# Performance work log

Measured on AMD Instinct MI355X. Metric: run time of the kernel, lower is better.

Reference implementation:

```python
import jax, jax.numpy as jnp
import numpy as np

B, H, S, DK = 2, 16, 2048, 128


def setup_inputs() -> dict:
    key = jax.random.key(0)
    kq, kk, kv = jax.random.split(key, 3)
    return {
        "queries": jax.random.normal(kq, (B, H, S, DK), dtype=jnp.float32),
        "keys": jax.random.normal(kk, (B, H, S, DK), dtype=jnp.float32),
        "values": jax.random.normal(kv, (B, H, S, DK), dtype=jnp.float32),
        "d_k": DK,
    }


def reference(queries, keys, values, d_k):
    # scores: [B, H, Sq, Sk] = Q @ K^T / sqrt(d_k)
    scale = 1.0 / np.sqrt(float(d_k)).astype(np.float32)
    scores = jnp.einsum("bhqd,bhkd->bhqk", queries, keys) * scale
    weights = jax.nn.softmax(scores, axis=-1)
    return jnp.einsum("bhqk,bhkd->bhqd", weights, values)
```

## Files before the change

kernel.cpp:

```cpp
#include <hip/hip_runtime.h>
#include <hip/hip_bf16.h>

#define SREF 2048
#define DHEAD 128
#define KVBLK 64
#define NTHREADS 256
#define NTILES (SREF / KVBLK)
#define PSTR 72
#define QSCALE 0.12751743f
#define THRLOG 8.0f

typedef short bf16x8 __attribute__((ext_vector_type(8)));
typedef float f32x4 __attribute__((ext_vector_type(4)));
typedef float f32x16 __attribute__((ext_vector_type(16)));

typedef const __attribute__((address_space(1))) void* gas_t;
typedef __attribute__((address_space(3))) void* las_t;

__device__ __forceinline__ ushort f2bf(float x) {
    unsigned u = __builtin_bit_cast(unsigned, x);
    u += 0x7fffu + ((u >> 16) & 1u);
    return (ushort)(u >> 16);
}

__device__ __forceinline__ float fexp2(float x) {
#if __has_builtin(__builtin_amdgcn_exp2f)
    return __builtin_amdgcn_exp2f(x);
#else
    return exp2f(x);
#endif
}

__device__ __forceinline__ unsigned cvtpk(float lo, float hi) {
    unsigned r;
    asm("v_cvt_pk_bf16_f32 %0, %1, %2" : "=v"(r) : "v"(lo), "v"(hi));
    return r;
}

__global__ __launch_bounds__(NTHREADS) void preconv_kernel(
    const float* __restrict__ K, const float* __restrict__ V,
    ushort* __restrict__ Kb, ushort* __restrict__ VTb)
{
    __shared__ ushort T[DHEAD * PSTR];
    const int t  = threadIdx.x;
    const int bh = blockIdx.y;
    const int s0 = blockIdx.x * KVBLK;
    const size_t base = (size_t)bh * SREF * DHEAD;

    const float* kb = K + base + (size_t)s0 * DHEAD;
    ushort* kout = Kb + base + (size_t)s0 * DHEAD;
    #pragma unroll
    for (int i = 0; i < 8; ++i) {
        int idx = t + i * NTHREADS;
        float4 f = *(const float4*)(kb + idx * 4);
        ushort4 h; h.x = f2bf(f.x); h.y = f2bf(f.y); h.z = f2bf(f.z); h.w = f2bf(f.w);
        *(ushort4*)(kout + idx * 4) = h;
    }

    const float* vb = V + base + (size_t)s0 * DHEAD;
    #pragma unroll
    for (int i = 0; i < 8; ++i) {
        const int key = (t & 31) + 32 * (i & 1);
        const int d4  = (t >> 5) + 8 * (i >> 1);
        float4 f = *(const float4*)(vb + key * DHEAD + d4 * 4);
        T[(d4 * 4 + 0) * PSTR + key] = f2bf(f.x);
        T[(d4 * 4 + 1) * PSTR + key] = f2bf(f.y);
        T[(d4 * 4 + 2) * PSTR + key] = f2bf(f.z);
        T[(d4 * 4 + 3) * PSTR + key] = f2bf(f.w);
    }
    __syncthreads();

    ushort* vt = VTb + (size_t)bh * DHEAD * SREF + s0;
    #pragma unroll
    for (int i = 0; i < 4; ++i) {
        int idx = t + i * NTHREADS;
        int d = idx >> 3;
        int c = (idx & 7) * 8;
        bf16x8 v = *(const bf16x8*)&T[d * PSTR + c];
        *(bf16x8*)(vt + (size_t)d * SREF + c) = v;
    }
}

__device__ __forceinline__ void softmax_step(
    f32x16& s0, f32x16& s1, float& mrun, float& lsumh,
    f32x16* acc, bf16x8* pa)
{
    float m0[8];
    #pragma unroll
    for (int i = 0; i < 8; ++i)
        m0[i] = fmaxf(fmaxf(s0[i], s0[i + 8]), fmaxf(s1[i], s1[i + 8]));
    float pmax = fmaxf(fmaxf(fmaxf(m0[0], m0[1]), fmaxf(m0[2], m0[3])),
                       fmaxf(fmaxf(m0[4], m0[5]), fmaxf(m0[6], m0[7])));
    pmax = fmaxf(pmax, __shfl_xor(pmax, 32));

    if (!__all(pmax <= mrun + THRLOG)) {
        const float mnew  = fmaxf(mrun, pmax);
        const float alpha = fexp2(mrun - mnew);
        mrun = mnew;
        lsumh *= alpha;
        #pragma unroll
        for (int db = 0; db < 4; ++db)
            #pragma unroll
            for (int i = 0; i < 16; ++i) acc[db][i] *= alpha;
    }

    float r0 = 0.f, r1 = 0.f, r2 = 0.f, r3 = 0.f;
    #pragma unroll
    for (int i = 0; i < 16; i += 4) {
        s0[i]   = fexp2(s0[i]   - mrun); r0 += s0[i];
        s0[i+1] = fexp2(s0[i+1] - mrun); r1 += s0[i+1];
        s0[i+2] = fexp2(s0[i+2] - mrun); r2 += s0[i+2];
        s0[i+3] = fexp2(s0[i+3] - mrun); r3 += s0[i+3];
    }
    #pragma unroll
    for (int i = 0; i < 16; i += 4) {
        s1[i]   = fexp2(s1[i]   - mrun); r0 += s1[i];
        s1[i+1] = fexp2(s1[i+1] - mrun); r1 += s1[i+1];
        s1[i+2] = fexp2(s1[i+2] - mrun); r2 += s1[i+2];
        s1[i+3] = fexp2(s1[i+3] - mrun); r3 += s1[i+3];
    }
    lsumh += (r0 + r1) + (r2 + r3);

    #pragma unroll
    for (int kb = 0; kb < 2; ++kb) {
        #pragma unroll
        for (int c = 0; c < 2; ++c) {
            unsigned x0, x1, y0, y1;
            if (kb == 0) {
                x0 = cvtpk(s0[8*c+0], s0[8*c+1]); x1 = cvtpk(s0[8*c+2], s0[8*c+3]);
                y0 = cvtpk(s0[8*c+4], s0[8*c+5]); y1 = cvtpk(s0[8*c+6], s0[8*c+7]);
            } else {
                x0 = cvtpk(s1[8*c+0], s1[8*c+1]); x1 = cvtpk(s1[8*c+2], s1[8*c+3]);
                y0 = cvtpk(s1[8*c+4], s1[8*c+5]); y1 = cvtpk(s1[8*c+6], s1[8*c+7]);
            }
            asm volatile("v_permlane32_swap_b32 %0, %1" : "+v"(x0), "+v"(y0));
            asm volatile("v_permlane32_swap_b32 %0, %1" : "+v"(x1), "+v"(y1));
            union { unsigned u[4]; bf16x8 v; } U;
            U.u[0] = x0; U.u[1] = x1; U.u[2] = y0; U.u[3] = y1;
            pa[kb * 2 + c] = U.v;
        }
    }
}

__global__ __launch_bounds__(NTHREADS, 2) void attn_fwd_kernel(
    const float* __restrict__ Q, const ushort* __restrict__ Kb,
    const ushort* __restrict__ VTb, float* __restrict__ O)
{
    __shared__ __align__(16) char smem[67584];

    const int t    = threadIdx.x;
    const int lane = t & 63;
    const int wv   = t >> 6;
    const int hi   = lane >> 5;
    const int q5   = lane & 31;
    const int swz  = (lane & 7) << 4;

    const int bh = blockIdx.y;
    const int q0 = blockIdx.x * 128;
    const size_t base = (size_t)bh * SREF * DHEAD;

    bf16x8 qf[8];
    {
        const float* qrow = Q + base + (size_t)(q0 + wv * 32 + q5) * DHEAD;
        #pragma unroll
        for (int dk = 0; dk < 8; ++dk) {
            const int d0 = dk * 16 + hi * 8;
            float4 a = *(const float4*)(qrow + d0);
            float4 b = *(const float4*)(qrow + d0 + 4);
            bf16x8 f;
            f[0] = (short)f2bf(a.x * QSCALE); f[1] = (short)f2bf(a.y * QSCALE);
            f[2] = (short)f2bf(a.z * QSCALE); f[3] = (short)f2bf(a.w * QSCALE);
            f[4] = (short)f2bf(b.x * QSCALE); f[5] = (short)f2bf(b.y * QSCALE);
            f[6] = (short)f2bf(b.z * QSCALE); f[7] = (short)f2bf(b.w * QSCALE);
            qf[dk] = f;
        }
    }

    const char* ksrcb = (const char*)(Kb + base);
    const char* vsrcb = (const char*)(VTb + (size_t)bh * DHEAD * SREF);

    const int kbaseL = q5 * 256 + ((hi * 16) ^ swz);
    const int vbaseL = q5 * 128 + ((hi * 16) ^ swz);

#define KOFF(b) ((b) * 16384)
#define VOFF(b) (32768 + (b) * 16384)

#define STAGE_K(b, kv0) do {                                                    \
    const char* kt_ = ksrcb + (size_t)(kv0) * (DHEAD * 2);                      \
    _Pragma("unroll")                                                           \
    for (int i_ = 0; i_ < 4; ++i_) {                                            \
        int L_ = t * 16 + i_ * 4096;                                            \
        int r_ = L_ >> 8;                                                       \
        __builtin_amdgcn_global_load_lds(                                       \
            (gas_t)(const void*)(kt_ + (L_ ^ ((r_ & 7) << 4))),                 \
            (las_t)(void*)(smem + KOFF(b) + L_), 16, 0, 0);                     \
    }                                                                           \
} while (0)

#define STAGE_V(b, kv0) do {                                                    \
    const char* vt_ = vsrcb + (size_t)(kv0) * 2;                                \
    _Pragma("unroll")                                                           \
    for (int i_ = 0; i_ < 4; ++i_) {                                            \
        int L_ = t * 16 + i_ * 4096;                                            \
        int d_ = L_ >> 7;                                                       \
        int c_ = L_ & 127;                                                      \
        __builtin_amdgcn_global_load_lds(                                       \
            (gas_t)(const void*)(vt_ + (size_t)d_ * (SREF * 2) + (c_ ^ ((d_ & 7) << 4))), \
            (las_t)(void*)(smem + VOFF(b) + L_), 16, 0, 0);                     \
    }                                                                           \
} while (0)

#define QK_REGION(sd0, sd1, kO_) do {                                           \
    _Pragma("unroll")                                                           \
    for (int i_ = 0; i_ < 16; ++i_) { sd0[i_] = 0.f; sd1[i_] = 0.f; }           \
    _Pragma("unroll")                                                           \
    for (int dk_ = 0; dk_ < 8; ++dk_) {                                         \
        bf16x8 kf0 = *(const bf16x8*)(smem + (kO_) + (kbaseL ^ (dk_ << 5)));    \
        sd0 = __builtin_amdgcn_mfma_f32_32x32x16_bf16(kf0, qf[dk_], sd0, 0, 0, 0); \
        bf16x8 kf1 = *(const bf16x8*)(smem + (kO_) + 8192 + (kbaseL ^ (dk_ << 5))); \
        sd1 = __builtin_amdgcn_mfma_f32_32x32x16_bf16(kf1, qf[dk_], sd1, 0, 0, 0); \
    }                                                                           \
} while (0)

#define PV_REGION(pa_, vO_) do {                                                \
    __builtin_amdgcn_s_setprio(1);                                              \
    _Pragma("unroll")                                                           \
    for (int db_ = 0; db_ < 4; ++db_) {                                         \
        _Pragma("unroll")                                                       \
        for (int ks_ = 0; ks_ < 4; ++ks_) {                                     \
            bf16x8 vf = *(const bf16x8*)(smem + (vO_) + db_ * 4096 + (vbaseL ^ (ks_ << 5))); \
            acc[db_] = __builtin_amdgcn_mfma_f32_32x32x16_bf16(vf, pa_[ks_], acc[db_], 0, 0, 0); \
        }                                                                       \
    }                                                                           \
    __builtin_amdgcn_s_setprio(0);                                              \
} while (0)

#define PHASE_SYNC() do {                                                       \
    asm volatile("s_waitcnt vmcnt(0)" ::: "memory");                            \
    __builtin_amdgcn_s_barrier();                                               \
    __builtin_amdgcn_sched_barrier(0);                                          \
} while (0)

    float mrun = -1e30f, lsumh = 0.0f;
    f32x16 acc[4];
    #pragma unroll
    for (int db = 0; db < 4; ++db)
        #pragma unroll
        for (int i = 0; i < 16; ++i) acc[db][i] = 0.0f;

    f32x16 sA0, sA1, sB0, sB1;
    bf16x8 pa[4];

    STAGE_K(0, 0);
    STAGE_K(1, KVBLK);
    STAGE_V(0, 0);
    asm volatile("s_waitcnt vmcnt(16)" ::: "memory");
    __builtin_amdgcn_s_barrier();
    __builtin_amdgcn_sched_barrier(0);
    QK_REGION(sA0, sA1, KOFF(0));

    for (int u = 0; u < 15; ++u) {
        const int t0 = 2 * u;
        PHASE_SYNC();
        STAGE_K(0, (t0 + 2) * KVBLK);
        STAGE_V(1, (t0 + 1) * KVBLK);
        softmax_step(sA0, sA1, mrun, lsumh, acc, pa);
        QK_REGION(sB0, sB1, KOFF(1));
        PV_REGION(pa, VOFF(0));
        PHASE_SYNC();
        STAGE_K(1, (t0 + 3) * KVBLK);
        STAGE_V(0, (t0 + 2) * KVBLK);
        softmax_step(sB0, sB1, mrun, lsumh, acc, pa);
        QK_REGION(sA0, sA1, KOFF(0));
        PV_REGION(pa, VOFF(1));
    }
    PHASE_SYNC();
    STAGE_V(1, 31 * KVBLK);
    softmax_step(sA0, sA1, mrun, lsumh, acc, pa);
    QK_REGION(sB0, sB1, KOFF(1));
    PV_REGION(pa, VOFF(0));
    PHASE_SYNC();
    softmax_step(sB0, sB1, mrun, lsumh, acc, pa);
    PV_REGION(pa, VOFF(1));

    __syncthreads();

    const float lsum = lsumh + __shfl_xor(lsumh, 32);
    const float inv  = 1.0f / lsum;
    const int eb = wv * 16896;
    #pragma unroll
    for (int db = 0; db < 4; ++db) {
        #pragma unroll
        for (int c = 0; c < 4; ++c) {
            f32x4 v;
            v[0] = acc[db][4*c+0] * inv;
            v[1] = acc[db][4*c+1] * inv;
            v[2] = acc[db][4*c+2] * inv;
            v[3] = acc[db][4*c+3] * inv;
            *(f32x4*)(smem + eb + q5 * 528 + db * 128 + c * 32 + hi * 16) = v;
        }
    }
    #pragma unroll
    for (int i = 0; i < 16; ++i) {
        const int flat  = lane + i * 64;
        const int row   = flat >> 5;
        const int chunk = flat & 31;
        f32x4 v = *(const f32x4*)(smem + eb + row * 528 + chunk * 16);
        *(f32x4*)(O + base + (size_t)(q0 + wv * 32 + row) * DHEAD + chunk * 4) = v;
    }
#undef STAGE_K
#undef STAGE_V
#undef QK_REGION
#undef PV_REGION
#undef PHASE_SYNC
#undef KOFF
#undef VOFF
}

__global__ __launch_bounds__(NTHREADS) void attn_fwd_fallback(
    const float* __restrict__ Q, const float* __restrict__ K,
    const float* __restrict__ V, float* __restrict__ O)
{
    __shared__ ushort Ksh[KVBLK * 136];
    __shared__ ushort Vsh[DHEAD * 72];
    __shared__ ushort Psh[4][16 * PSTR];

    const int t    = threadIdx.x;
    const int lane = t & 63;
    const int wv   = t >> 6;
    const int lq   = lane & 15;
    const int kh   = lane >> 4;

    const int bh = blockIdx.y;
    const int q0 = blockIdx.x * 64;
    const size_t base = (size_t)bh * SREF * DHEAD;

    const float scale = 0.08838834764831845f;
    bf16x8 qf[4];
    {
        const float* qrow = Q + base + (size_t)(q0 + wv * 16 + lq) * DHEAD;
        #pragma unroll
        for (int kk = 0; kk < 4; ++kk) {
            const int d0 = kk * 32 + kh * 8;
            float4 a = *(const float4*)(qrow + d0);
            float4 b = *(const float4*)(qrow + d0 + 4);
            bf16x8 f;
            f[0] = (short)f2bf(a.x * scale); f[1] = (short)f2bf(a.y * scale);
            f[2] = (short)f2bf(a.z * scale); f[3] = (short)f2bf(a.w * scale);
            f[4] = (short)f2bf(b.x * scale); f[5] = (short)f2bf(b.y * scale);
            f[6] = (short)f2bf(b.z * scale); f[7] = (short)f2bf(b.w * scale);
            qf[kk] = f;
        }
    }

    float mrun[4], lrun[4];
    f32x4 acc_o[8];
    #pragma unroll
    for (int r = 0; r < 4; ++r) { mrun[r] = -1e30f; lrun[r] = 0.0f; }
    #pragma unroll
    for (int db = 0; db < 8; ++db) acc_o[db] = (f32x4){0.f, 0.f, 0.f, 0.f};

    for (int kv0 = 0; kv0 < SREF; kv0 += KVBLK) {
        __syncthreads();
        const float* kbase = K + base + (size_t)kv0 * DHEAD;
        #pragma unroll
        for (int i = 0; i < 8; ++i) {
            const int idx = t + i * NTHREADS;
            const int row = idx >> 5;
            const int c4  = idx & 31;
            float4 f = *(const float4*)(kbase + row * DHEAD + c4 * 4);
            ushort4 h;
            h.x = f2bf(f.x); h.y = f2bf(f.y); h.z = f2bf(f.z); h.w = f2bf(f.w);
            *(ushort4*)&Ksh[row * 136 + c4 * 4] = h;
        }
        const float* vbase = V + base + (size_t)kv0 * DHEAD;
        #pragma unroll
        for (int i = 0; i < 8; ++i) {
            const int key = (t & 31) + 32 * (i & 1);
            const int d4  = (t >> 5) + 8 * (i >> 1);
            float4 f = *(const float4*)(vbase + key * DHEAD + d4 * 4);
            Vsh[(d4 * 4 + 0) * 72 + key] = f2bf(f.x);
            Vsh[(d4 * 4 + 1) * 72 + key] = f2bf(f.y);
            Vsh[(d4 * 4 + 2) * 72 + key] = f2bf(f.z);
            Vsh[(d4 * 4 + 3) * 72 + key] = f2bf(f.w);
        }
        __syncthreads();

        f32x4 accs[4];
        #pragma unroll
        for (int nb = 0; nb < 4; ++nb) accs[nb] = (f32x4){0.f, 0.f, 0.f, 0.f};
        #pragma unroll
        for (int kk = 0; kk < 4; ++kk) {
            #pragma unroll
            for (int nb = 0; nb < 4; ++nb) {
                bf16x8 kf = *(const bf16x8*)&Ksh[(nb * 16 + lq) * 136 + kk * 32 + kh * 8];
                accs[nb] = __builtin_amdgcn_mfma_f32_16x16x32_bf16(qf[kk], kf, accs[nb], 0, 0, 0);
            }
        }

        float ps[4][4];
        #pragma unroll
        for (int r = 0; r < 4; ++r) {
            float v = fmaxf(fmaxf(accs[0][r], accs[1][r]), fmaxf(accs[2][r], accs[3][r]));
            #pragma unroll
            for (int mk = 1; mk < 16; mk <<= 1) v = fmaxf(v, __shfl_xor(v, mk));
            const float mnew  = fmaxf(mrun[r], v);
            const float alpha = __expf(mrun[r] - mnew);
            mrun[r] = mnew;
            float rs = 0.0f;
            #pragma unroll
            for (int nb = 0; nb < 4; ++nb) {
                const float p = __expf(accs[nb][r] - mnew);
                ps[nb][r] = p;
                rs += p;
            }
            #pragma unroll
            for (int mk = 1; mk < 16; mk <<= 1) rs += __shfl_xor(rs, mk);
            lrun[r] = lrun[r] * alpha + rs;
            #pragma unroll
            for (int db = 0; db < 8; ++db) acc_o[db][r] *= alpha;
        }

        #pragma unroll
        for (int nb = 0; nb < 4; ++nb)
            #pragma unroll
            for (int r = 0; r < 4; ++r)
                Psh[wv][(kh * 4 + r) * PSTR + nb * 16 + lq] = f2bf(ps[nb][r]);

        #pragma unroll
        for (int ks = 0; ks < 2; ++ks) {
            bf16x8 pa = *(const bf16x8*)&Psh[wv][lq * PSTR + ks * 32 + kh * 8];
            #pragma unroll
            for (int db = 0; db < 8; ++db) {
                bf16x8 vf = *(const bf16x8*)&Vsh[(db * 16 + lq) * 72 + ks * 32 + kh * 8];
                acc_o[db] = __builtin_amdgcn_mfma_f32_16x16x32_bf16(pa, vf, acc_o[db], 0, 0, 0);
            }
        }
    }

    #pragma unroll
    for (int r = 0; r < 4; ++r) {
        const float inv = 1.0f / lrun[r];
        float* orow = O + base + (size_t)(q0 + wv * 16 + kh * 4 + r) * DHEAD;
        #pragma unroll
        for (int db = 0; db < 8; ++db)
            orow[db * 16 + lq] = acc_o[db][r] * inv;
    }
}

extern "C" void kernel_launch(void* const* d_in, const int* in_sizes, int n_in,
                              void* d_out, int out_size, void* d_ws, size_t ws_size,
                              hipStream_t stream) {
    const float* Q = (const float*)d_in[0];
    const float* K = (const float*)d_in[1];
    const float* V = (const float*)d_in[2];
    float* O = (float*)d_out;
    const int BH = in_sizes[0] / (SREF * DHEAD);
    const size_t nel = (size_t)BH * SREF * DHEAD;

    if (ws_size >= 2 * nel * sizeof(ushort)) {
        ushort* Kb  = (ushort*)d_ws;
        ushort* VTb = Kb + nel;
        preconv_kernel<<<dim3(SREF / KVBLK, BH), NTHREADS, 0, stream>>>(K, V, Kb, VTb);
        attn_fwd_kernel<<<dim3(SREF / 128, BH), NTHREADS, 0, stream>>>(Q, Kb, VTb, O);
    } else {
        attn_fwd_fallback<<<dim3(SREF / 64, BH), NTHREADS, 0, stream>>>(Q, K, V, O);
    }
}
```

Before: 104.4 us.

## Restructure attention kernel into 8-wave ping-pong with two wave groups

The main attention kernel goes from 4 waves handling 128 queries to 8 waves handling 256 queries, split into two groups of four. While one group runs its QK and PV matrix work, the other runs softmax, and barriers swap the roles. This aims to overlap MFMA work with softmax exponentials and to halve K/V staging traffic per query. The LDS layout changes to a 16-row swizzle with interleaved V, the grid order becomes (BH, seq) for better L2 locality, and the epilogue is serialized into three rounds because LDS is shrunk. In exchange, register pressure at 512 threads is higher and the grid has fewer blocks, which may hurt occupancy.

```diff
diff --git a/kernel.cpp b/kernel.cpp
--- a/kernel.cpp
+++ b/kernel.cpp
@@ -5,7 +5,8 @@
 #define DHEAD 128
 #define KVBLK 64
 #define NTHREADS 256
-#define NTILES (SREF / KVBLK)
+#define ATHREADS 512
+#define NT (SREF / KVBLK)
 #define PSTR 72
 #define QSCALE 0.12751743f
 #define THRLOG 8.0f
@@ -44,7 +45,7 @@
     __shared__ ushort T[DHEAD * PSTR];
     const int t  = threadIdx.x;
     const int bh = blockIdx.y;
-    const int s0 = blockIdx.x * KVBLK;
+    const int s0 = blockIdx.x * 64;
     const size_t base = (size_t)bh * SREF * DHEAD;
 
     const float* kb = K + base + (size_t)s0 * DHEAD;
@@ -142,21 +143,22 @@
     }
 }
 
-__global__ __launch_bounds__(NTHREADS, 2) void attn_fwd_kernel(
+__global__ __launch_bounds__(ATHREADS, 2) void attn_fwd_kernel(
     const float* __restrict__ Q, const ushort* __restrict__ Kb,
     const ushort* __restrict__ VTb, float* __restrict__ O)
 {
-    __shared__ __align__(16) char smem[67584];
+    __shared__ __align__(16) char smem[65536];
 
     const int t    = threadIdx.x;
     const int lane = t & 63;
     const int wv   = t >> 6;
+    const int g    = wv >> 2;
     const int hi   = lane >> 5;
     const int q5   = lane & 31;
-    const int swz  = (lane & 7) << 4;
-
-    const int bh = blockIdx.y;
-    const int q0 = blockIdx.x * 128;
+    const int sw   = (q5 & 15) << 4;
+
+    const int bh = blockIdx.x;
+    const int q0 = blockIdx.y * 256;
     const size_t base = (size_t)bh * SREF * DHEAD;
 
     bf16x8 qf[8];
@@ -179,67 +181,68 @@
     const char* ksrcb = (const char*)(Kb + base);
     const char* vsrcb = (const char*)(VTb + (size_t)bh * DHEAD * SREF);
 
-    const int kbaseL = q5 * 256 + ((hi * 16) ^ swz);
-    const int vbaseL = q5 * 128 + ((hi * 16) ^ swz);
-
-#define KOFF(b) ((b) * 16384)
-#define VOFF(b) (32768 + (b) * 16384)
-
-#define STAGE_K(b, kv0) do {                                                    \
-    const char* kt_ = ksrcb + (size_t)(kv0) * (DHEAD * 2);                      \
+    const int kread = q5 * 256 + ((hi * 16) ^ sw);
+    const int vread = q5 * 256 + ((hi * 16) ^ sw);
+
+#define STAGE_K(tt) do {                                                        \
+    const char* kt_ = ksrcb + (size_t)(tt) * 16384;                             \
     _Pragma("unroll")                                                           \
-    for (int i_ = 0; i_ < 4; ++i_) {                                            \
-        int L_ = t * 16 + i_ * 4096;                                            \
+    for (int i_ = 0; i_ < 2; ++i_) {                                            \
+        int L_ = t * 16 + i_ * 8192;                                            \
         int r_ = L_ >> 8;                                                       \
         __builtin_amdgcn_global_load_lds(                                       \
-            (gas_t)(const void*)(kt_ + (L_ ^ ((r_ & 7) << 4))),                 \
-            (las_t)(void*)(smem + KOFF(b) + L_), 16, 0, 0);                     \
+            (gas_t)(const void*)(kt_ + (L_ ^ ((r_ & 15) << 4))),                \
+            (las_t)(void*)(smem + ((tt) & 1) * 16384 + L_), 16, 0, 0);          \
     }                                                                           \
 } while (0)
 
-#define STAGE_V(b, kv0) do {                                                    \
-    const char* vt_ = vsrcb + (size_t)(kv0) * 2;                                \
+#define STAGE_V(tt) do {                                                        \
+    const char* vt_ = vsrcb + (size_t)(tt) * 128;                               \
     _Pragma("unroll")                                                           \
-    for (int i_ = 0; i_ < 4; ++i_) {                                            \
-        int L_ = t * 16 + i_ * 4096;                                            \
-        int d_ = L_ >> 7;                                                       \
-        int c_ = L_ & 127;                                                      \
+    for (int i_ = 0; i_ < 2; ++i_) {                                            \
+        int L_ = t * 16 + i_ * 8192;                                            \
+        int r_ = L_ >> 8;                                                       \
+        int offp_ = (L_ & 255) ^ ((r_ & 15) << 4);                              \
+        int d_ = r_ + 64 * (offp_ >> 7);                                        \
         __builtin_amdgcn_global_load_lds(                                       \
-            (gas_t)(const void*)(vt_ + (size_t)d_ * (SREF * 2) + (c_ ^ ((d_ & 7) << 4))), \
-            (las_t)(void*)(smem + VOFF(b) + L_), 16, 0, 0);                     \
+            (gas_t)(const void*)(vt_ + (size_t)d_ * (SREF * 2) + (offp_ & 127)),\
+            (las_t)(void*)(smem + 32768 + ((tt) & 1) * 16384 + L_), 16, 0, 0);  \
     }                                                                           \
 } while (0)
 
-#define QK_REGION(sd0, sd1, kO_) do {                                           \
+#define QK(tt) do {                                                             \
+    const int kO_ = ((tt) & 1) * 16384;                                         \
     _Pragma("unroll")                                                           \
-    for (int i_ = 0; i_ < 16; ++i_) { sd0[i_] = 0.f; sd1[i_] = 0.f; }           \
+    for (int i_ = 0; i_ < 16; ++i_) { s0[i_] = 0.f; s1[i_] = 0.f; }             \
+    __builtin_amdgcn_s_setprio(1);                                              \
     _Pragma("unroll")                                                           \
     for (int dk_ = 0; dk_ < 8; ++dk_) {                                         \
-        bf16x8 kf0 = *(const bf16x8*)(smem + (kO_) + (kbaseL ^ (dk_ << 5)));    \
-        sd0 = __builtin_amdgcn_mfma_f32_32x32x16_bf16(kf0, qf[dk_], sd0, 0, 0, 0); \
-        bf16x8 kf1 = *(const bf16x8*)(smem + (kO_) + 8192 + (kbaseL ^ (dk_ << 5))); \
-        sd1 = __builtin_amdgcn_mfma_f32_32x32x16_bf16(kf1, qf[dk_], sd1, 0, 0, 0); \
+        const int off_ = kread ^ (dk_ << 5);                                    \
+        bf16x8 kf0 = *(const bf16x8*)(smem + kO_ + off_);                       \
+        s0 = __builtin_amdgcn_mfma_f32_32x32x16_bf16(kf0, qf[dk_], s0, 0, 0, 0);\
+        bf16x8 kf1 = *(const bf16x8*)(smem + kO_ + 8192 + off_);                \
+        s1 = __builtin_amdgcn_mfma_f32_32x32x16_bf16(kf1, qf[dk_], s1, 0, 0, 0);\
     }                                                                           \
+    __builtin_amdgcn_s_setprio(0);                                              \
 } while (0)
 
-#define PV_REGION(pa_, vO_) do {                                                \
+#define PV(tt) do {                                                             \
+    const int vO_ = 32768 + ((tt) & 1) * 16384;                                 \
     __builtin_amdgcn_s_setprio(1);                                              \
     _Pragma("unroll")                                                           \
     for (int db_ = 0; db_ < 4; ++db_) {                                         \
+        const int vb_ = vread + (db_ & 1) * 8192;                               \
         _Pragma("unroll")                                                       \
         for (int ks_ = 0; ks_ < 4; ++ks_) {                                     \
-            bf16x8 vf = *(const bf16x8*)(smem + (vO_) + db_ * 4096 + (vbaseL ^ (ks_ << 5))); \
-            acc[db_] = __builtin_amdgcn_mfma_f32_32x32x16_bf16(vf, pa_[ks_], acc[db_], 0, 0, 0); \
+            bf16x8 vf = *(const bf16x8*)(smem + vO_ +                           \
+                (vb_ ^ (ks_ << 5) ^ ((db_ >> 1) << 7)));                        \
+            acc[db_] = __builtin_amdgcn_mfma_f32_32x32x16_bf16(vf, pa[ks_], acc[db_], 0, 0, 0); \
         }                                                                       \
     }                                                                           \
     __builtin_amdgcn_s_setprio(0);                                              \
 } while (0)
 
-#define PHASE_SYNC() do {                                                       \
-    asm volatile("s_waitcnt vmcnt(0)" ::: "memory");                            \
-    __builtin_amdgcn_s_barrier();                                               \
-    __builtin_amdgcn_sched_barrier(0);                                          \
-} while (0)
+#define BAR() do { __builtin_amdgcn_s_barrier(); __builtin_amdgcn_sched_barrier(0); } while (0)
 
     float mrun = -1e30f, lsumh = 0.0f;
     f32x16 acc[4];
@@ -248,80 +251,83 @@
         #pragma unroll
         for (int i = 0; i < 16; ++i) acc[db][i] = 0.0f;
 
-    f32x16 sA0, sA1, sB0, sB1;
+    f32x16 s0, s1;
     bf16x8 pa[4];
 
-    STAGE_K(0, 0);
-    STAGE_K(1, KVBLK);
-    STAGE_V(0, 0);
-    asm volatile("s_waitcnt vmcnt(16)" ::: "memory");
-    __builtin_amdgcn_s_barrier();
-    __builtin_amdgcn_sched_barrier(0);
-    QK_REGION(sA0, sA1, KOFF(0));
-
-    for (int u = 0; u < 15; ++u) {
-        const int t0 = 2 * u;
-        PHASE_SYNC();
-        STAGE_K(0, (t0 + 2) * KVBLK);
-        STAGE_V(1, (t0 + 1) * KVBLK);
-        softmax_step(sA0, sA1, mrun, lsumh, acc, pa);
-        QK_REGION(sB0, sB1, KOFF(1));
-        PV_REGION(pa, VOFF(0));
-        PHASE_SYNC();
-        STAGE_K(1, (t0 + 3) * KVBLK);
-        STAGE_V(0, (t0 + 2) * KVBLK);
-        softmax_step(sB0, sB1, mrun, lsumh, acc, pa);
-        QK_REGION(sA0, sA1, KOFF(0));
-        PV_REGION(pa, VOFF(1));
-    }
-    PHASE_SYNC();
-    STAGE_V(1, 31 * KVBLK);
-    softmax_step(sA0, sA1, mrun, lsumh, acc, pa);
-    QK_REGION(sB0, sB1, KOFF(1));
-    PV_REGION(pa, VOFF(0));
-    PHASE_SYNC();
-    softmax_step(sB0, sB1, mrun, lsumh, acc, pa);
-    PV_REGION(pa, VOFF(1));
+    STAGE_K(0);
+    asm volatile("s_waitcnt vmcnt(0)" ::: "memory");
+    BAR();
+
+    STAGE_K(1);
+    STAGE_V(0);
+    if (g == 0) { QK(0); }
+    BAR();
+    if (g == 0) { softmax_step(s0, s1, mrun, lsumh, acc, pa); }
+    else        { QK(0); }
+    asm volatile("s_waitcnt vmcnt(0)" ::: "memory");
+    BAR();
+
+    #pragma unroll 1
+    for (int tt = 1; tt < NT; ++tt) {
+        if (tt + 1 < NT) STAGE_K(tt + 1);
+        STAGE_V(tt);
+        if (g == 0) { PV(tt - 1); QK(tt); }
+        else        { softmax_step(s0, s1, mrun, lsumh, acc, pa); }
+        BAR();
+        if (g == 0) { softmax_step(s0, s1, mrun, lsumh, acc, pa); }
+        else        { PV(tt - 1); QK(tt); }
+        asm volatile("s_waitcnt vmcnt(0)" ::: "memory");
+        BAR();
+    }
+
+    if (g == 0) { PV(NT - 1); }
+    else        { softmax_step(s0, s1, mrun, lsumh, acc, pa); }
+    BAR();
+    if (g == 1) { PV(NT - 1); }
 
     __syncthreads();
-
     const float lsum = lsumh + __shfl_xor(lsumh, 32);
     const float inv  = 1.0f / lsum;
-    const int eb = wv * 16896;
-    #pragma unroll
-    for (int db = 0; db < 4; ++db) {
-        #pragma unroll
-        for (int c = 0; c < 4; ++c) {
-            f32x4 v;
-            v[0] = acc[db][4*c+0] * inv;
-            v[1] = acc[db][4*c+1] * inv;
-            v[2] = acc[db][4*c+2] * inv;
-            v[3] = acc[db][4*c+3] * inv;
-            *(f32x4*)(smem + eb + q5 * 528 + db * 128 + c * 32 + hi * 16) = v;
-        }
-    }
-    #pragma unroll
-    for (int i = 0; i < 16; ++i) {
-        const int flat  = lane + i * 64;
-        const int row   = flat >> 5;
-        const int chunk = flat & 31;
-        f32x4 v = *(const f32x4*)(smem + eb + row * 528 + chunk * 16);
-        *(f32x4*)(O + base + (size_t)(q0 + wv * 32 + row) * DHEAD + chunk * 4) = v;
+
+    #pragma unroll
+    for (int round = 0; round < 3; ++round) {
+        if (wv / 3 == round) {
+            const int eb = (wv % 3) * 16896;
+            #pragma unroll
+            for (int db = 0; db < 4; ++db) {
+                #pragma unroll
+                for (int c = 0; c < 4; ++c) {
+                    f32x4 v;
+                    v[0] = acc[db][4*c+0] * inv;
+                    v[1] = acc[db][4*c+1] * inv;
+                    v[2] = acc[db][4*c+2] * inv;
+                    v[3] = acc[db][4*c+3] * inv;
+                    *(f32x4*)(smem + eb + q5 * 528 + db * 128 + c * 32 + hi * 16) = v;
+                }
+            }
+            #pragma unroll
+            for (int i = 0; i < 16; ++i) {
+                const int flat  = lane + i * 64;
+                const int row   = flat >> 5;
+                const int chunk = flat & 31;
+                f32x4 v = *(const f32x4*)(smem + eb + row * 528 + chunk * 16);
+                *(f32x4*)(O + base + (size_t)(q0 + wv * 32 + row) * DHEAD + chunk * 4) = v;
+            }
+        }
+        __syncthreads();
     }
 #undef STAGE_K
 #undef STAGE_V
-#undef QK_REGION
-#undef PV_REGION
-#undef PHASE_SYNC
-#undef KOFF
-#undef VOFF
+#undef QK
+#undef PV
+#undef BAR
 }
 
 __global__ __launch_bounds__(NTHREADS) void attn_fwd_fallback(
     const float* __restrict__ Q, const float* __restrict__ K,
     const float* __restrict__ V, float* __restrict__ O)
 {
-    __shared__ ushort Ksh[KVBLK * 136];
+    __shared__ ushort Ksh[64 * 136];
     __shared__ ushort Vsh[DHEAD * 72];
     __shared__ ushort Psh[4][16 * PSTR];
 
@@ -360,7 +366,7 @@
     #pragma unroll
     for (int db = 0; db < 8; ++db) acc_o[db] = (f32x4){0.f, 0.f, 0.f, 0.f};
 
-    for (int kv0 = 0; kv0 < SREF; kv0 += KVBLK) {
+    for (int kv0 = 0; kv0 < SREF; kv0 += 64) {
         __syncthreads();
         const float* kbase = K + base + (size_t)kv0 * DHEAD;
         #pragma unroll
@@ -461,8 +467,8 @@
     if (ws_size >= 2 * nel * sizeof(ushort)) {
         ushort* Kb  = (ushort*)d_ws;
         ushort* VTb = Kb + nel;
-        preconv_kernel<<<dim3(SREF / KVBLK, BH), NTHREADS, 0, stream>>>(K, V, Kb, VTb);
-        attn_fwd_kernel<<<dim3(SREF / 128, BH), NTHREADS, 0, stream>>>(Q, Kb, VTb, O);
+        preconv_kernel<<<dim3(SREF / 64, BH), NTHREADS, 0, stream>>>(K, V, Kb, VTb);
+        attn_fwd_kernel<<<dim3(BH, SREF / 256), ATHREADS, 0, stream>>>(Q, Kb, VTb, O);
     } else {
         attn_fwd_fallback<<<dim3(SREF / 64, BH), NTHREADS, 0, stream>>>(Q, K, V, O);
     }
```

Result: faster. 98.59 us (-5.5%).
